# Optimization experiments

Hardware: AMD Instinct MI355X
Metric: run time of the kernel (lower is better)

Reference implementation:

```python
import jax, jax.numpy as jnp
import numpy as np

SEQ_LEN = 256
NLAYERS = 3
H = 128  # latent_dim == input_dim
OUT_DIM = 2
BATCH = 1024


def setup_inputs() -> dict:
    key = jax.random.key(0)
    ks = jax.random.split(key, 7)
    s = 1.0 / np.sqrt(H)  # PyTorch RNN init scale
    return {
        "hiddens": jax.random.normal(ks[0], (BATCH, NLAYERS, H), jnp.float32),
        "W_ih": jax.random.uniform(ks[1], (NLAYERS, 3 * H, H), jnp.float32, -s, s),
        "W_hh": jax.random.uniform(ks[2], (NLAYERS, 3 * H, H), jnp.float32, -s, s),
        "b_ih": jax.random.uniform(ks[3], (NLAYERS, 3 * H), jnp.float32, -s, s),
        "b_hh": jax.random.uniform(ks[4], (NLAYERS, 3 * H), jnp.float32, -s, s),
        "fc_w": jax.random.uniform(ks[5], (OUT_DIM, H), jnp.float32, -s, s),
        "fc_b": jax.random.uniform(ks[6], (OUT_DIM,), jnp.float32, -s, s),
    }


def _gru_cell(x, h, w_ih, w_hh, bi, bh):
    # x, h: [B, H]; w_*: [3H, H]; b_*: [3H]; PyTorch gate order (r, z, n)
    gx = x @ w_ih.T + bi          # [B, 3H]
    gh = h @ w_hh.T + bh          # [B, 3H]
    xr, xz, xn = jnp.split(gx, 3, axis=-1)
    hr, hz, hn = jnp.split(gh, 3, axis=-1)
    r = jax.nn.sigmoid(xr + hr)
    z = jax.nn.sigmoid(xz + hz)
    n = jnp.tanh(xn + r * hn)
    return (1.0 - z) * n + z * h


def reference(hiddens, W_ih, W_hh, b_ih, b_hh, fc_w, fc_b):
    # hiddens: [B, L, H] -> layer-major [L, B, H] (torch transposes 0,1)
    h = jnp.transpose(hiddens, (1, 0, 2))
    B = hiddens.shape[0]
    x0 = jnp.zeros((B, H), hiddens.dtype)  # torch.zeros initial input

    def step(carry, _):
        x, h = carry
        new_h = []
        inp = x
        for l in range(NLAYERS):
            hl = _gru_cell(inp, h[l], W_ih[l], W_hh[l], b_ih[l], b_hh[l])
            new_h.append(hl)
            inp = hl  # top-layer output feeds next layer / next step
        return (inp, jnp.stack(new_h)), inp

    (_, _), outs = jax.lax.scan(step, (x0, h), None, length=SEQ_LEN)
    outs = jnp.transpose(outs, (1, 0, 2))        # [B, T, H]
    return outs @ fc_w.T + fc_b                  # [B, T, out_dim]
```

## Files before the change

kernel.cpp:

```cpp
#include <hip/hip_runtime.h>
#include <stdint.h>

typedef int   v4i __attribute__((ext_vector_type(4)));
typedef float v4f __attribute__((ext_vector_type(4)));

#define ACT_OFF  65536
#define SLOT_SZ  13824
#define LO_OFF   6912
#define FC_OFF   (ACT_OFF + 2*SLOT_SZ)
#define SMEM_SZ  (FC_OFF + 2048)

#define QW   1436.84056f
#define C1f  4.38394754e-5f
#define C2f  3.45193507e-7f

__device__ __forceinline__ float sigm(float x) {
  return __builtin_amdgcn_rcpf(1.f + __expf(-x));
}
__device__ __forceinline__ float tanh_(float x) {
  return 1.f - 2.f * __builtin_amdgcn_rcpf(1.f + __expf(2.f * x));
}

__global__ void prep_weights(const float* __restrict__ Wih,
                             const float* __restrict__ Whh,
                             int8_t* __restrict__ img) {
  int bid = blockIdx.x, lane = threadIdx.x;
  int w = bid / 36, blk = bid % 36;
  int l = blk / 12, rem = blk % 12, o = rem >> 1, kh = rem & 1;
  const float* M = (o & 1) ? Whh : Wih;
  int row = (o >> 1) * 128 + w * 16 + (lane & 15);
  int k0 = kh * 64 + (lane >> 4) * 16;
  const float* src = M + l * 49152 + row * 128 + k0;
  int words[4];
  #pragma unroll
  for (int j4 = 0; j4 < 4; ++j4) {
    unsigned wd = 0;
    #pragma unroll
    for (int j = 0; j < 4; ++j) {
      int q = (int)rintf(src[j4 * 4 + j] * QW);
      wd |= ((unsigned)(q & 255)) << (8 * j);
    }
    words[j4] = (int)wd;
  }
  *(v4i*)(img + (((long)bid) * 64 + lane) * 16) = *(const v4i*)words;
}

__global__ __launch_bounds__(512, 2)
void gru_main(const float* __restrict__ hiddens, const float* __restrict__ bih,
              const float* __restrict__ bhh, const float* __restrict__ fcw,
              const float* __restrict__ fcb, const int8_t* __restrict__ img,
              float* __restrict__ out) {
  extern __shared__ char smem[];
  const int tid = threadIdx.x, wg = blockIdx.x;
  const int lane = tid & 63, w = tid >> 6, col = lane & 15, q = lane >> 4;
  const int hid = w * 16 + col;

  v4i wr[28];
  #pragma unroll
  for (int i = 0; i < 28; ++i) {
    int blk = (i < 24) ? ((i >> 3) * 12 + (i & 7)) : (i + 8);
    wr[i] = *(const v4i*)(img + (((long)(w * 36 + blk)) * 64 + lane) * 16);
  }
  #pragma unroll
  for (int j = 0; j < 8; ++j) {
    int blk = (j >> 2) * 12 + 8 + (j & 3);
    *(v4i*)(smem + w * 8192 + j * 1024 + lane * 16) =
        *(const v4i*)(img + (((long)(w * 36 + blk)) * 64 + lane) * 16);
  }
  if (tid < 128) {
    int kh = tid >> 6, ln = tid & 63, c2 = ln & 15, q2 = ln >> 4;
    int words[4] = {0, 0, 0, 0};
    if (c2 < 2) {
      const float* src = fcw + c2 * 128 + kh * 64 + q2 * 16;
      #pragma unroll
      for (int j4 = 0; j4 < 4; ++j4) {
        unsigned wd = 0;
        #pragma unroll
        for (int j = 0; j < 4; ++j) {
          int qv = (int)rintf(src[j4 * 4 + j] * QW);
          wd |= ((unsigned)(qv & 255)) << (8 * j);
        }
        words[j4] = (int)wd;
      }
    }
    *(v4i*)(smem + FC_OFF + kh * 1024 + ln * 16) = *(const v4i*)words;
  }
  float bR[3], bZ[3], bNX[3], bNH[3];
  v4f hst[3];
  #pragma unroll
  for (int l = 0; l < 3; ++l) {
    bR[l]  = bih[l * 384 + hid]       + bhh[l * 384 + hid];
    bZ[l]  = bih[l * 384 + 128 + hid] + bhh[l * 384 + 128 + hid];
    bNX[l] = bih[l * 384 + 256 + hid];
    bNH[l] = bhh[l * 384 + 256 + hid];
    int8_t* ew0 = (int8_t*)(smem + ACT_OFF + l * 2304 + q * 576 + hid);
    #pragma unroll
    for (int r = 0; r < 4; ++r) {
      float v = hiddens[((long)(wg * 16 + q * 4 + r)) * 384 + l * 128 + hid];
      hst[l][r] = v;
      float f = v * 15.875f, fhi = rintf(f);
      ew0[r * 144]          = (int8_t)(int)fhi;
      ew0[r * 144 + LO_OFF] = (int8_t)(int)rintf((f - fhi) * 127.0f);
    }
  }
  float myfcb = (w == 0 && col < 2) ? fcb[col] : 0.f;
  __syncthreads();

  const char* fragb = smem + ACT_OFF + col * 144 + q * 16;
  char* ewb = smem + ACT_OFF + q * 576 + hid;

  #pragma unroll 1
  for (int t = 0; t < 256; ++t) {
    const int so = (t & 1) * SLOT_SZ;
    const int sn = SLOT_SZ - so;
    #pragma unroll
    for (int l = 0; l < 3; ++l) {
      v4i aRh = {0,0,0,0}, aRl = {0,0,0,0}, aZh = {0,0,0,0}, aZl = {0,0,0,0};
      v4i aXh = {0,0,0,0}, aXl = {0,0,0,0}, aHh = {0,0,0,0}, aHl = {0,0,0,0};
      if (l > 0 || t > 0) {
        const char* xp = fragb + ((l == 0) ? (so + 2 * 2304) : (sn + (l - 1) * 2304));
        #pragma unroll
        for (int kh = 0; kh < 2; ++kh) {
          v4i xh = *(const v4i*)(xp + kh * 64);
          v4i xl = *(const v4i*)(xp + kh * 64 + LO_OFF);
          v4i wrx = wr[(l < 2 ? l * 8 : 16) + kh];
          v4i wzx = wr[(l < 2 ? l * 8 : 16) + 4 + kh];
          v4i wnx = (l < 2) ? *(const v4i*)(smem + w * 8192 + (l * 4 + kh) * 1024 + lane * 16)
                            : wr[24 + kh];
          aRh = __builtin_amdgcn_mfma_i32_16x16x64_i8(xh, wrx, aRh, 0, 0, 0);
          aRl = __builtin_amdgcn_mfma_i32_16x16x64_i8(xl, wrx, aRl, 0, 0, 0);
          aZh = __builtin_amdgcn_mfma_i32_16x16x64_i8(xh, wzx, aZh, 0, 0, 0);
          aZl = __builtin_amdgcn_mfma_i32_16x16x64_i8(xl, wzx, aZl, 0, 0, 0);
          aXh = __builtin_amdgcn_mfma_i32_16x16x64_i8(xh, wnx, aXh, 0, 0, 0);
          aXl = __builtin_amdgcn_mfma_i32_16x16x64_i8(xl, wnx, aXl, 0, 0, 0);
        }
      }
      {
        const char* hp = fragb + so + l * 2304;
        #pragma unroll
        for (int kh = 0; kh < 2; ++kh) {
          v4i hh = *(const v4i*)(hp + kh * 64);
          v4i hl = *(const v4i*)(hp + kh * 64 + LO_OFF);
          v4i wrh = wr[(l < 2 ? l * 8 : 16) + 2 + kh];
          v4i wzh = wr[(l < 2 ? l * 8 : 16) + 6 + kh];
          v4i wnh = (l < 2) ? *(const v4i*)(smem + w * 8192 + (l * 4 + 2 + kh) * 1024 + lane * 16)
                            : wr[26 + kh];
          aRh = __builtin_amdgcn_mfma_i32_16x16x64_i8(hh, wrh, aRh, 0, 0, 0);
          aRl = __builtin_amdgcn_mfma_i32_16x16x64_i8(hl, wrh, aRl, 0, 0, 0);
          aZh = __builtin_amdgcn_mfma_i32_16x16x64_i8(hh, wzh, aZh, 0, 0, 0);
          aZl = __builtin_amdgcn_mfma_i32_16x16x64_i8(hl, wzh, aZl, 0, 0, 0);
          aHh = __builtin_amdgcn_mfma_i32_16x16x64_i8(hh, wnh, aHh, 0, 0, 0);
          aHl = __builtin_amdgcn_mfma_i32_16x16x64_i8(hl, wnh, aHl, 0, 0, 0);
        }
      }
      int8_t* ew = (int8_t*)(ewb + sn + l * 2304);
      #pragma unroll
      for (int r = 0; r < 4; ++r) {
        float gR = bR[l] + C1f * (float)aRh[r] + C2f * (float)aRl[r];
        float gZ = bZ[l] + C1f * (float)aZh[r] + C2f * (float)aZl[r];
        float gX = bNX[l] + C1f * (float)aXh[r] + C2f * (float)aXl[r];
        float gH = bNH[l] + C1f * (float)aHh[r] + C2f * (float)aHl[r];
        float rg = sigm(gR), zg = sigm(gZ);
        float ng = tanh_(gX + rg * gH);
        float hn = ng + zg * (hst[l][r] - ng);
        hst[l][r] = hn;
        float f = hn * 15.875f, fhi = rintf(f);
        ew[r * 144]          = (int8_t)(int)fhi;
        ew[r * 144 + LO_OFF] = (int8_t)(int)rintf((f - fhi) * 127.0f);
      }
      __syncthreads();
    }
    if (w == 0) {
      v4i dh = {0,0,0,0}, dl = {0,0,0,0};
      const char* xp = fragb + sn + 2 * 2304;
      #pragma unroll
      for (int kh = 0; kh < 2; ++kh) {
        v4i xh = *(const v4i*)(xp + kh * 64);
        v4i xl = *(const v4i*)(xp + kh * 64 + LO_OFF);
        v4i fw = *(const v4i*)(smem + FC_OFF + kh * 1024 + lane * 16);
        dh = __builtin_amdgcn_mfma_i32_16x16x64_i8(xh, fw, dh, 0, 0, 0);
        dl = __builtin_amdgcn_mfma_i32_16x16x64_i8(xl, fw, dl, 0, 0, 0);
      }
      if (col < 2) {
        #pragma unroll
        for (int r = 0; r < 4; ++r)
          out[((long)(wg * 16 + q * 4 + r) * 256 + t) * 2 + col] =
              myfcb + C1f * (float)dh[r] + C2f * (float)dl[r];
      }
    }
  }
}

extern "C" void kernel_launch(void* const* d_in, const int* in_sizes, int n_in,
                              void* d_out, int out_size, void* d_ws, size_t ws_size,
                              hipStream_t stream) {
  (void)in_sizes; (void)n_in; (void)out_size; (void)ws_size;
  const float* hiddens = (const float*)d_in[0];
  const float* Wih     = (const float*)d_in[1];
  const float* Whh     = (const float*)d_in[2];
  const float* bih     = (const float*)d_in[3];
  const float* bhh     = (const float*)d_in[4];
  const float* fcw     = (const float*)d_in[5];
  const float* fcb     = (const float*)d_in[6];
  int8_t* img = (int8_t*)d_ws;
  float* out = (float*)d_out;

  hipFuncSetAttribute(reinterpret_cast<const void*>(gru_main),
                      hipFuncAttributeMaxDynamicSharedMemorySize, SMEM_SZ);

  prep_weights<<<288, 64, 0, stream>>>(Wih, Whh, img);
  gru_main<<<64, 512, SMEM_SZ, stream>>>(hiddens, bih, bhh, fcw, fcb, img, out);
}
```

Baseline: 884.9 us.

## Keep all GRU weights in registers and transpose MFMA operands for packed stores

The kernel now holds every weight block in registers (36 v4i per lane) instead of staging some n-gate weights in LDS. It swaps the MFMA operand order so each lane's output covers 4 consecutive hidden units, which lets the new int8 hi/lo activations be packed and written as one 32-bit store per lane instead of eight byte stores. Biases move to LDS and are read as vectors, the layer-2 fragment is reused across steps, and the FC output is written as float2. The aim is to cut LDS traffic and weight reloads on the serial recurrence path, at the cost of heavy register pressure under the 512x2 launch bound, which risks spilling.

```diff
diff --git a/kernel.cpp b/kernel.cpp
--- a/kernel.cpp
+++ b/kernel.cpp
@@ -4,10 +4,10 @@
 typedef int   v4i __attribute__((ext_vector_type(4)));
 typedef float v4f __attribute__((ext_vector_type(4)));
 
-#define ACT_OFF  65536
 #define SLOT_SZ  13824
 #define LO_OFF   6912
-#define FC_OFF   (ACT_OFF + 2*SLOT_SZ)
+#define BIAS_OFF (2*SLOT_SZ)
+#define FC_OFF   (BIAS_OFF + 6144)
 #define SMEM_SZ  (FC_OFF + 2048)
 
 #define QW   1436.84056f
@@ -45,6 +45,16 @@
   *(v4i*)(img + (((long)bid) * 64 + lane) * 16) = *(const v4i*)words;
 }
 
+__device__ __forceinline__ unsigned pack_hi(const float* f, const float* fhi) {
+  unsigned wd = 0;
+  #pragma unroll
+  for (int r = 0; r < 4; ++r) {
+    int v = (int)fhi[r];
+    wd |= ((unsigned)(v & 255)) << (8 * r);
+  }
+  return wd;
+}
+
 __global__ __launch_bounds__(512, 2)
 void gru_main(const float* __restrict__ hiddens, const float* __restrict__ bih,
               const float* __restrict__ bhh, const float* __restrict__ fcw,
@@ -53,20 +63,12 @@
   extern __shared__ char smem[];
   const int tid = threadIdx.x, wg = blockIdx.x;
   const int lane = tid & 63, w = tid >> 6, col = lane & 15, q = lane >> 4;
-  const int hid = w * 16 + col;
-
-  v4i wr[28];
-  #pragma unroll
-  for (int i = 0; i < 28; ++i) {
-    int blk = (i < 24) ? ((i >> 3) * 12 + (i & 7)) : (i + 8);
-    wr[i] = *(const v4i*)(img + (((long)(w * 36 + blk)) * 64 + lane) * 16);
-  }
-  #pragma unroll
-  for (int j = 0; j < 8; ++j) {
-    int blk = (j >> 2) * 12 + 8 + (j & 3);
-    *(v4i*)(smem + w * 8192 + j * 1024 + lane * 16) =
-        *(const v4i*)(img + (((long)(w * 36 + blk)) * 64 + lane) * 16);
-  }
+
+  v4i wr[36];
+  #pragma unroll
+  for (int i = 0; i < 36; ++i)
+    wr[i] = *(const v4i*)(img + (((long)(w * 36 + i)) * 64 + lane) * 16);
+
   if (tid < 128) {
     int kh = tid >> 6, ln = tid & 63, c2 = ln & 15, q2 = ln >> 4;
     int words[4] = {0, 0, 0, 0};
@@ -85,29 +87,37 @@
     }
     *(v4i*)(smem + FC_OFF + kh * 1024 + ln * 16) = *(const v4i*)words;
   }
-  float bR[3], bZ[3], bNX[3], bNH[3];
+  for (int i = tid; i < 1536; i += 512) {
+    int l = i >> 9, type = (i >> 7) & 3, h = i & 127;
+    float bv;
+    if      (type == 0) bv = bih[l * 384 + h]       + bhh[l * 384 + h];
+    else if (type == 1) bv = bih[l * 384 + 128 + h] + bhh[l * 384 + 128 + h];
+    else if (type == 2) bv = bih[l * 384 + 256 + h];
+    else                bv = bhh[l * 384 + 256 + h];
+    *(float*)(smem + BIAS_OFF + i * 4) = bv;
+  }
+  for (int i = tid; i < 6144; i += 512) {
+    int l = i >> 11, b = (i >> 7) & 15, h = i & 127;
+    float v = hiddens[((long)(wg * 16 + b)) * 384 + l * 128 + h];
+    float f = v * 15.875f, fhi = rintf(f);
+    *(int8_t*)(smem + l * 2304 + b * 144 + h)          = (int8_t)(int)fhi;
+    *(int8_t*)(smem + l * 2304 + b * 144 + h + LO_OFF) = (int8_t)(int)rintf((f - fhi) * 127.f);
+  }
   v4f hst[3];
   #pragma unroll
-  for (int l = 0; l < 3; ++l) {
-    bR[l]  = bih[l * 384 + hid]       + bhh[l * 384 + hid];
-    bZ[l]  = bih[l * 384 + 128 + hid] + bhh[l * 384 + 128 + hid];
-    bNX[l] = bih[l * 384 + 256 + hid];
-    bNH[l] = bhh[l * 384 + 256 + hid];
-    int8_t* ew0 = (int8_t*)(smem + ACT_OFF + l * 2304 + q * 576 + hid);
+  for (int l = 0; l < 3; ++l)
     #pragma unroll
-    for (int r = 0; r < 4; ++r) {
-      float v = hiddens[((long)(wg * 16 + q * 4 + r)) * 384 + l * 128 + hid];
-      hst[l][r] = v;
-      float f = v * 15.875f, fhi = rintf(f);
-      ew0[r * 144]          = (int8_t)(int)fhi;
-      ew0[r * 144 + LO_OFF] = (int8_t)(int)rintf((f - fhi) * 127.0f);
-    }
-  }
-  float myfcb = (w == 0 && col < 2) ? fcb[col] : 0.f;
+    for (int r = 0; r < 4; ++r)
+      hst[l][r] = hiddens[((long)(wg * 16 + col)) * 384 + l * 128 + w * 16 + q * 4 + r];
+
+  const float fcb0 = fcb[0], fcb1 = fcb[1];
   __syncthreads();
 
-  const char* fragb = smem + ACT_OFF + col * 144 + q * 16;
-  char* ewb = smem + ACT_OFF + q * 576 + hid;
+  const char* fragb = smem + col * 144 + q * 16;
+  char* ewb = smem + col * 144 + w * 16 + q * 4;
+  const char* biasb = smem + BIAS_OFF + (w * 16 + q * 4) * 4;
+
+  v4i c2h[2], c2l[2];
 
   #pragma unroll 1
   for (int t = 0; t < 256; ++t) {
@@ -118,74 +128,81 @@
       v4i aRh = {0,0,0,0}, aRl = {0,0,0,0}, aZh = {0,0,0,0}, aZl = {0,0,0,0};
       v4i aXh = {0,0,0,0}, aXl = {0,0,0,0}, aHh = {0,0,0,0}, aHl = {0,0,0,0};
       if (l > 0 || t > 0) {
-        const char* xp = fragb + ((l == 0) ? (so + 2 * 2304) : (sn + (l - 1) * 2304));
         #pragma unroll
         for (int kh = 0; kh < 2; ++kh) {
-          v4i xh = *(const v4i*)(xp + kh * 64);
-          v4i xl = *(const v4i*)(xp + kh * 64 + LO_OFF);
-          v4i wrx = wr[(l < 2 ? l * 8 : 16) + kh];
-          v4i wzx = wr[(l < 2 ? l * 8 : 16) + 4 + kh];
-          v4i wnx = (l < 2) ? *(const v4i*)(smem + w * 8192 + (l * 4 + kh) * 1024 + lane * 16)
-                            : wr[24 + kh];
-          aRh = __builtin_amdgcn_mfma_i32_16x16x64_i8(xh, wrx, aRh, 0, 0, 0);
-          aRl = __builtin_amdgcn_mfma_i32_16x16x64_i8(xl, wrx, aRl, 0, 0, 0);
-          aZh = __builtin_amdgcn_mfma_i32_16x16x64_i8(xh, wzx, aZh, 0, 0, 0);
-          aZl = __builtin_amdgcn_mfma_i32_16x16x64_i8(xl, wzx, aZl, 0, 0, 0);
-          aXh = __builtin_amdgcn_mfma_i32_16x16x64_i8(xh, wnx, aXh, 0, 0, 0);
-          aXl = __builtin_amdgcn_mfma_i32_16x16x64_i8(xl, wnx, aXl, 0, 0, 0);
+          v4i xh, xl;
+          if (l == 0) {
+            xh = *(const v4i*)(fragb + so + 2 * 2304 + kh * 64);
+            xl = *(const v4i*)(fragb + so + 2 * 2304 + kh * 64 + LO_OFF);
+            c2h[kh] = xh; c2l[kh] = xl;
+          } else {
+            xh = *(const v4i*)(fragb + sn + (l - 1) * 2304 + kh * 64);
+            xl = *(const v4i*)(fragb + sn + (l - 1) * 2304 + kh * 64 + LO_OFF);
+          }
+          aRh = __builtin_amdgcn_mfma_i32_16x16x64_i8(wr[l*12 + 0 + kh], xh, aRh, 0, 0, 0);
+          aRl = __builtin_amdgcn_mfma_i32_16x16x64_i8(wr[l*12 + 0 + kh], xl, aRl, 0, 0, 0);
+          aZh = __builtin_amdgcn_mfma_i32_16x16x64_i8(wr[l*12 + 4 + kh], xh, aZh, 0, 0, 0);
+          aZl = __builtin_amdgcn_mfma_i32_16x16x64_i8(wr[l*12 + 4 + kh], xl, aZl, 0, 0, 0);
+          aXh = __builtin_amdgcn_mfma_i32_16x16x64_i8(wr[l*12 + 8 + kh], xh, aXh, 0, 0, 0);
+          aXl = __builtin_amdgcn_mfma_i32_16x16x64_i8(wr[l*12 + 8 + kh], xl, aXl, 0, 0, 0);
         }
       }
-      {
-        const char* hp = fragb + so + l * 2304;
-        #pragma unroll
-        for (int kh = 0; kh < 2; ++kh) {
-          v4i hh = *(const v4i*)(hp + kh * 64);
-          v4i hl = *(const v4i*)(hp + kh * 64 + LO_OFF);
-          v4i wrh = wr[(l < 2 ? l * 8 : 16) + 2 + kh];
-          v4i wzh = wr[(l < 2 ? l * 8 : 16) + 6 + kh];
-          v4i wnh = (l < 2) ? *(const v4i*)(smem + w * 8192 + (l * 4 + 2 + kh) * 1024 + lane * 16)
-                            : wr[26 + kh];
-          aRh = __builtin_amdgcn_mfma_i32_16x16x64_i8(hh, wrh, aRh, 0, 0, 0);
-          aRl = __builtin_amdgcn_mfma_i32_16x16x64_i8(hl, wrh, aRl, 0, 0, 0);
-          aZh = __builtin_amdgcn_mfma_i32_16x16x64_i8(hh, wzh, aZh, 0, 0, 0);
-          aZl = __builtin_amdgcn_mfma_i32_16x16x64_i8(hl, wzh, aZl, 0, 0, 0);
-          aHh = __builtin_amdgcn_mfma_i32_16x16x64_i8(hh, wnh, aHh, 0, 0, 0);
-          aHl = __builtin_amdgcn_mfma_i32_16x16x64_i8(hl, wnh, aHl, 0, 0, 0);
+      #pragma unroll
+      for (int kh = 0; kh < 2; ++kh) {
+        v4i hh, hl;
+        if (l == 2) {
+          if (t == 0) { c2h[kh] = *(const v4i*)(fragb + so + 2 * 2304 + kh * 64);
+                        c2l[kh] = *(const v4i*)(fragb + so + 2 * 2304 + kh * 64 + LO_OFF); }
+          hh = c2h[kh]; hl = c2l[kh];
+        } else {
+          hh = *(const v4i*)(fragb + so + l * 2304 + kh * 64);
+          hl = *(const v4i*)(fragb + so + l * 2304 + kh * 64 + LO_OFF);
         }
-      }
-      int8_t* ew = (int8_t*)(ewb + sn + l * 2304);
+        aRh = __builtin_amdgcn_mfma_i32_16x16x64_i8(wr[l*12 + 2 + kh], hh, aRh, 0, 0, 0);
+        aRl = __builtin_amdgcn_mfma_i32_16x16x64_i8(wr[l*12 + 2 + kh], hl, aRl, 0, 0, 0);
+        aZh = __builtin_amdgcn_mfma_i32_16x16x64_i8(wr[l*12 + 6 + kh], hh, aZh, 0, 0, 0);
+        aZl = __builtin_amdgcn_mfma_i32_16x16x64_i8(wr[l*12 + 6 + kh], hl, aZl, 0, 0, 0);
+        aHh = __builtin_amdgcn_mfma_i32_16x16x64_i8(wr[l*12 + 10 + kh], hh, aHh, 0, 0, 0);
+        aHl = __builtin_amdgcn_mfma_i32_16x16x64_i8(wr[l*12 + 10 + kh], hl, aHl, 0, 0, 0);
+      }
+      v4f bRv = *(const v4f*)(biasb + (l * 4 + 0) * 512);
+      v4f bZv = *(const v4f*)(biasb + (l * 4 + 1) * 512);
+      v4f bXv = *(const v4f*)(biasb + (l * 4 + 2) * 512);
+      v4f bHv = *(const v4f*)(biasb + (l * 4 + 3) * 512);
+      unsigned hiw = 0, low = 0;
       #pragma unroll
       for (int r = 0; r < 4; ++r) {
-        float gR = bR[l] + C1f * (float)aRh[r] + C2f * (float)aRl[r];
-        float gZ = bZ[l] + C1f * (float)aZh[r] + C2f * (float)aZl[r];
-        float gX = bNX[l] + C1f * (float)aXh[r] + C2f * (float)aXl[r];
-        float gH = bNH[l] + C1f * (float)aHh[r] + C2f * (float)aHl[r];
+        float gR = bRv[r] + C1f * (float)aRh[r] + C2f * (float)aRl[r];
+        float gZ = bZv[r] + C1f * (float)aZh[r] + C2f * (float)aZl[r];
+        float gX = bXv[r] + C1f * (float)aXh[r] + C2f * (float)aXl[r];
+        float gH = bHv[r] + C1f * (float)aHh[r] + C2f * (float)aHl[r];
         float rg = sigm(gR), zg = sigm(gZ);
         float ng = tanh_(gX + rg * gH);
         float hn = ng + zg * (hst[l][r] - ng);
         hst[l][r] = hn;
         float f = hn * 15.875f, fhi = rintf(f);
-        ew[r * 144]          = (int8_t)(int)fhi;
-        ew[r * 144 + LO_OFF] = (int8_t)(int)rintf((f - fhi) * 127.0f);
-      }
+        hiw |= ((unsigned)(((int)fhi) & 255)) << (8 * r);
+        low |= ((unsigned)(((int)rintf((f - fhi) * 127.f)) & 255)) << (8 * r);
+      }
+      *(unsigned*)(ewb + sn + l * 2304)          = hiw;
+      *(unsigned*)(ewb + sn + l * 2304 + LO_OFF) = low;
       __syncthreads();
     }
     if (w == 0) {
       v4i dh = {0,0,0,0}, dl = {0,0,0,0};
-      const char* xp = fragb + sn + 2 * 2304;
       #pragma unroll
       for (int kh = 0; kh < 2; ++kh) {
-        v4i xh = *(const v4i*)(xp + kh * 64);
-        v4i xl = *(const v4i*)(xp + kh * 64 + LO_OFF);
+        v4i xh = *(const v4i*)(fragb + sn + 2 * 2304 + kh * 64);
+        v4i xl = *(const v4i*)(fragb + sn + 2 * 2304 + kh * 64 + LO_OFF);
         v4i fw = *(const v4i*)(smem + FC_OFF + kh * 1024 + lane * 16);
-        dh = __builtin_amdgcn_mfma_i32_16x16x64_i8(xh, fw, dh, 0, 0, 0);
-        dl = __builtin_amdgcn_mfma_i32_16x16x64_i8(xl, fw, dl, 0, 0, 0);
-      }
-      if (col < 2) {
-        #pragma unroll
-        for (int r = 0; r < 4; ++r)
-          out[((long)(wg * 16 + q * 4 + r) * 256 + t) * 2 + col] =
-              myfcb + C1f * (float)dh[r] + C2f * (float)dl[r];
+        dh = __builtin_amdgcn_mfma_i32_16x16x64_i8(fw, xh, dh, 0, 0, 0);
+        dl = __builtin_amdgcn_mfma_i32_16x16x64_i8(fw, xl, dl, 0, 0, 0);
+      }
+      if (q == 0) {
+        float2 o2;
+        o2.x = fcb0 + C1f * (float)dh[0] + C2f * (float)dl[0];
+        o2.y = fcb1 + C1f * (float)dh[1] + C2f * (float)dl[1];
+        *(float2*)(out + (((long)(wg * 16 + col)) * 256 + t) * 2) = o2;
       }
     }
   }
@@ -205,9 +222,6 @@
   int8_t* img = (int8_t*)d_ws;
   float* out = (float*)d_out;
 
-  hipFuncSetAttribute(reinterpret_cast<const void*>(gru_main),
-                      hipFuncAttributeMaxDynamicSharedMemorySize, SMEM_SZ);
-
   prep_weights<<<288, 64, 0, stream>>>(Wih, Whh, img);
   gru_main<<<64, 512, SMEM_SZ, stream>>>(hiddens, bih, bhh, fcw, fcb, img, out);
 }
```

Measured after the change: 900.6 us. No clear change (+1.8%).
